# Kernel optimization log

Measured on AMD Instinct MI355X. Metric: run time of the kernel, lower is better.

Reference implementation:

```python
import jax, jax.numpy as jnp
import numpy as np

B, QN, KVN = 4, 512, 512
QD, KD, H, VD = 512, 512, 256, 256


def setup_inputs() -> dict:
    key = jax.random.key(0)
    ks = jax.random.split(key, 6)
    q = jax.random.normal(ks[0], (B, QN, QD), dtype=jnp.float32)
    k = jax.random.normal(ks[1], (B, KVN, KD), dtype=jnp.float32)
    v = jax.random.normal(ks[2], (B, KVN, VD), dtype=jnp.float32)
    # Linear weights (torch nn.Linear stores [out, in]; bias=False)
    Wq = jax.random.normal(ks[3], (H, QD), dtype=jnp.float32) / np.sqrt(QD)
    Wk = jax.random.normal(ks[4], (H, KD), dtype=jnp.float32) / np.sqrt(KD)
    wv = jax.random.normal(ks[5], (H,), dtype=jnp.float32) / np.sqrt(H)
    return {"q": q, "k": k, "v": v, "Wq": Wq, "Wk": Wk, "wv": wv}


def reference(q, k, v, Wq, Wk, wv):
    # Project queries and keys to hidden dim H
    qh = jnp.einsum("bqd,hd->bqh", q, Wq)  # [B, QN, H]
    kh = jnp.einsum("bkd,hd->bkh", k, Wk)  # [B, KVN, H]
    # Broadcast add + tanh: [B, QN, KVN, H]
    energy = jnp.tanh(qh[:, :, None, :] + kh[:, None, :, :])
    # Score projection to scalar per (q, kv) pair
    scores = jnp.einsum("bqkh,h->bqk", energy, wv)  # [B, QN, KVN]
    attention = jax.nn.softmax(scores, axis=-1)
    # Dropout omitted (inference mode)
    output = jnp.einsum("bqk,bkv->bqv", attention, v)  # [B, QN, VD]
    return (output, attention)
```

## Files before the change

### kernel.cpp

```cpp
#include <hip/hip_runtime.h>

#define B_ 4
#define QN 512
#define KVN 512
#define QD_ 512
#define H_ 256
#define VD_ 256
#define TOTR 2048

typedef __attribute__((ext_vector_type(8))) short bf16x8;
typedef __attribute__((ext_vector_type(4))) float f32x4;
typedef __attribute__((ext_vector_type(4))) unsigned short u16x4;
typedef unsigned short u16;

__device__ __forceinline__ float rcp_(float x) { return __builtin_amdgcn_rcpf(x); }
__device__ __forceinline__ float ex2_(float x) { return __builtin_amdgcn_exp2f(x); }

__device__ __forceinline__ u16 bf16_rne(float x) {
    unsigned u = __float_as_uint(x);
    unsigned r = u + 0x7FFFu + ((u >> 16) & 1u);
    return (u16)(r >> 16);
}
__device__ __forceinline__ void split2(float x, u16& h, u16& l) {
    h = bf16_rne(x);
    float hf = __uint_as_float((unsigned)h << 16);
    l = bf16_rne(x - hf);
}
__device__ __forceinline__ void split4(float4 a, u16x4& h, u16x4& l) {
    u16 hh, ll;
    split2(a.x, hh, ll); h[0] = hh; l[0] = ll;
    split2(a.y, hh, ll); h[1] = hh; l[1] = ll;
    split2(a.z, hh, ll); h[2] = hh; l[2] = ll;
    split2(a.w, hh, ll); h[3] = hh; l[3] = ll;
}

__global__ __launch_bounds__(256) void prep(const float* __restrict__ q,
                                            const float* __restrict__ k,
                                            const float* __restrict__ Wq,
                                            const float* __restrict__ Wk,
                                            const float* __restrict__ v,
                                            const float* __restrict__ wv,
                                            u16* __restrict__ q_hi, u16* __restrict__ q_lo,
                                            u16* __restrict__ k_hi, u16* __restrict__ k_lo,
                                            u16* __restrict__ w_hi, u16* __restrict__ w_lo,
                                            u16* __restrict__ vt_hi, u16* __restrict__ vt_lo,
                                            float* __restrict__ iwg) {
    __shared__ float ts[64][65];
    const int tid = threadIdx.x;
    if (blockIdx.x < 2304) {
        const int NQ = 2048 * 512 / 4, NW = 256 * 512 / 4;
        int idx = blockIdx.x * 256 + tid;
        const float* src; u16 *dh, *dl; int off;
        if (idx < NQ)               { src = q;  dh = q_hi; dl = q_lo; off = idx; }
        else if (idx < 2 * NQ)      { src = k;  dh = k_hi; dl = k_lo; off = idx - NQ; }
        else if (idx < 2 * NQ + NW) { src = Wq; dh = w_hi; dl = w_lo; off = idx - 2 * NQ; }
        else { src = Wk; dh = w_hi + 256 * 512; dl = w_lo + 256 * 512; off = idx - 2 * NQ - NW; }
        float4 v4 = ((const float4*)src)[off];
        u16x4 h, l;
        split4(v4, h, l);
        *(u16x4*)(dh + off * 4) = h;
        *(u16x4*)(dl + off * 4) = l;
    } else if (blockIdx.x < 2432) {
        int bid = blockIdx.x - 2304;
        int j0 = (bid & 7) * 64, n0 = ((bid >> 3) & 3) * 64, b = bid >> 5;
#pragma unroll
        for (int t = 0; t < 4; ++t) {
            int idx = t * 256 + tid;
            int j = idx >> 4, nq = idx & 15;
            float4 v4 = *(const float4*)(v + ((size_t)b * KVN + j0 + j) * VD_ + n0 + nq * 4);
            *(float4*)&ts[j][nq * 4] = v4;
        }
        __syncthreads();
#pragma unroll
        for (int t = 0; t < 4; ++t) {
            int idx = t * 256 + tid;
            int jq = idx & 15, n = idx >> 4;
            u16x4 h, l;
            u16 hh, ll;
#pragma unroll
            for (int e = 0; e < 4; ++e) {
                split2(ts[jq * 4 + e][n], hh, ll);
                h[e] = hh; l[e] = ll;
            }
            size_t off = ((size_t)b * VD_ + n0 + n) * KVN + j0 + jq * 4;
            *(u16x4*)(vt_hi + off) = h;
            *(u16x4*)(vt_lo + off) = l;
        }
    } else {
        iwg[tid] = rcp_(wv[tid]);
    }
}

__global__ __launch_bounds__(256) void proj_mfma(const u16* __restrict__ q_hi, const u16* __restrict__ q_lo,
                                                 const u16* __restrict__ k_hi, const u16* __restrict__ k_lo,
                                                 const u16* __restrict__ w_hi, const u16* __restrict__ w_lo,
                                                 const float* __restrict__ iwg,
                                                 float* __restrict__ eqw, float* __restrict__ ekT) {
    const int z = blockIdx.z;
    const u16* __restrict__ Ah_g = z ? k_hi : q_hi;
    const u16* __restrict__ Al_g = z ? k_lo : q_lo;
    const u16* __restrict__ Bh_g = w_hi + (size_t)z * H_ * QD_;
    const u16* __restrict__ Bl_g = w_lo + (size_t)z * H_ * QD_;
    __shared__ u16 Ash[4][32][8], Asl[4][32][8], Bsh[4][32][8], Bsl[4][32][8];
    const int tid = threadIdx.x;
    const int wave = tid >> 6, lane = tid & 63;
    const int fl = lane & 15, kg = lane >> 4;
    const int r0 = blockIdx.y * 32, c0 = blockIdx.x * 32;
    const int ar = 16 * (wave & 1), bc = 16 * (wave >> 1);
    const int frow = (tid & 127) >> 2, fkq = tid & 3, fsel = tid >> 7;
    f32x4 acc = {};
    for (int k0 = 0; k0 < QD_; k0 += 32) {
        __syncthreads();
        {
            const u16* as = (fsel ? Al_g : Ah_g) + (size_t)(r0 + frow) * QD_ + k0 + fkq * 8;
            u16* ad = fsel ? &Asl[fkq][frow][0] : &Ash[fkq][frow][0];
            *(uint4*)ad = *(const uint4*)as;
            const u16* bs = (fsel ? Bl_g : Bh_g) + (size_t)(c0 + frow) * QD_ + k0 + fkq * 8;
            u16* bd = fsel ? &Bsl[fkq][frow][0] : &Bsh[fkq][frow][0];
            *(uint4*)bd = *(const uint4*)bs;
        }
        __syncthreads();
        bf16x8 a_h = *(const bf16x8*)&Ash[kg][ar + fl][0];
        bf16x8 a_l = *(const bf16x8*)&Asl[kg][ar + fl][0];
        bf16x8 b_h = *(const bf16x8*)&Bsh[kg][bc + fl][0];
        bf16x8 b_l = *(const bf16x8*)&Bsl[kg][bc + fl][0];
        acc = __builtin_amdgcn_mfma_f32_16x16x32_bf16(a_h, b_h, acc, 0, 0, 0);
        acc = __builtin_amdgcn_mfma_f32_16x16x32_bf16(a_h, b_l, acc, 0, 0, 0);
        acc = __builtin_amdgcn_mfma_f32_16x16x32_bf16(a_l, b_h, acc, 0, 0, 0);
    }
    const float cs = 2.8853900817779268f;
    const int rg = kg * 4;
    if (z == 1) {
        float4 o = {ex2_(acc[0] * cs), ex2_(acc[1] * cs), ex2_(acc[2] * cs), ex2_(acc[3] * cs)};
        *(float4*)(ekT + (size_t)(c0 + bc + fl) * TOTR + r0 + ar + rg) = o;
    } else {
        float iw = iwg[c0 + bc + fl];
#pragma unroll
        for (int r = 0; r < 4; ++r)
            eqw[(size_t)(r0 + ar + rg + r) * H_ + c0 + bc + fl] = ex2_(acc[r] * cs) * iw;
    }
}

__global__ __launch_bounds__(512, 4) void scores_sm(const float* __restrict__ eqw,
                                                    const float* __restrict__ ekT,
                                                    const float* __restrict__ iwg,
                                                    float* __restrict__ attn,
                                                    u16* __restrict__ at_hi,
                                                    u16* __restrict__ at_lo) {
    const int tid = threadIdx.x;
    const int row0 = blockIdx.x * 4;
    const int b = row0 >> 9;
    const int colg = b * KVN + tid;
    float sc[4] = {};
#pragma unroll 2
    for (int ch = 0; ch < 16; ++ch) {
        const int h0 = ch * 16;
        float ekr[16];
#pragma unroll
        for (int t = 0; t < 16; ++t)
            ekr[t] = ekT[(size_t)(h0 + t) * TOTR + colg];
        float4 iw4[4];
#pragma unroll
        for (int g = 0; g < 4; ++g) iw4[g] = *(const float4*)(iwg + h0 + 4 * g);
#pragma unroll
        for (int qq = 0; qq < 4; ++qq) {
            const float* ep = eqw + (size_t)(row0 + qq) * H_ + h0;
            float s = 0.f;
#pragma unroll
            for (int g = 0; g < 4; ++g) {
                float4 e = *(const float4*)(ep + 4 * g);
                float d0 = __builtin_fmaf(ekr[4 * g + 0], e.x, iw4[g].x);
                float d1 = __builtin_fmaf(ekr[4 * g + 1], e.y, iw4[g].y);
                float d2 = __builtin_fmaf(ekr[4 * g + 2], e.z, iw4[g].z);
                float d3 = __builtin_fmaf(ekr[4 * g + 3], e.w, iw4[g].w);
                float ab = d0 * d1, cd = d2 * d3;
                float num = __builtin_fmaf(d0 + d1, cd, (d2 + d3) * ab);
                s = __builtin_fmaf(num, rcp_(ab * cd), s);
            }
            sc[qq] += s;
        }
    }
    __shared__ float red[8][4];
    const int wid = tid >> 6, lane = tid & 63;
    float ev[4];
#pragma unroll
    for (int qq = 0; qq < 4; ++qq)
        ev[qq] = ex2_(sc[qq] * -2.8853900817779268f);
#pragma unroll
    for (int qq = 0; qq < 4; ++qq) {
        float ssum = ev[qq];
#pragma unroll
        for (int d = 1; d < 64; d <<= 1) ssum += __shfl_xor(ssum, d);
        if (lane == 0) red[wid][qq] = ssum;
    }
    __syncthreads();
#pragma unroll
    for (int qq = 0; qq < 4; ++qq) {
        float tot = ((red[0][qq] + red[1][qq]) + (red[2][qq] + red[3][qq])) +
                    ((red[4][qq] + red[5][qq]) + (red[6][qq] + red[7][qq]));
        float a = ev[qq] * rcp_(tot);
        size_t base = (size_t)(row0 + qq) * KVN + tid;
        attn[base] = a;
        u16 h, l;
        split2(a, h, l);
        at_hi[base] = h;
        at_lo[base] = l;
    }
}

__global__ __launch_bounds__(256) void out_mfma(const u16* __restrict__ vt_hi, const u16* __restrict__ vt_lo,
                                                const u16* __restrict__ at_hi, const u16* __restrict__ at_lo,
                                                float* __restrict__ out) {
    const int b = blockIdx.z;
    const u16* __restrict__ Ah_g = vt_hi + (size_t)b * VD_ * KVN;
    const u16* __restrict__ Al_g = vt_lo + (size_t)b * VD_ * KVN;
    const u16* __restrict__ Bh_g = at_hi + (size_t)b * QN * KVN;
    const u16* __restrict__ Bl_g = at_lo + (size_t)b * QN * KVN;
    float* __restrict__ outb = out + (size_t)b * QN * VD_;
    __shared__ u16 Ash[4][32][8], Asl[4][32][8], Bsh[4][32][8], Bsl[4][32][8];
    const int tid = threadIdx.x;
    const int wave = tid >> 6, lane = tid & 63;
    const int fl = lane & 15, kg = lane >> 4;
    const int r0 = blockIdx.y * 32;
    const int c0 = blockIdx.x * 32;
    const int ar = 16 * (wave & 1), bc = 16 * (wave >> 1);
    const int frow = (tid & 127) >> 2, fkq = tid & 3, fsel = tid >> 7;
    f32x4 acc = {};
    for (int k0 = 0; k0 < KVN; k0 += 32) {
        __syncthreads();
        {
            const u16* as = (fsel ? Al_g : Ah_g) + (size_t)(r0 + frow) * KVN + k0 + fkq * 8;
            u16* ad = fsel ? &Asl[fkq][frow][0] : &Ash[fkq][frow][0];
            *(uint4*)ad = *(const uint4*)as;
            const u16* bs = (fsel ? Bl_g : Bh_g) + (size_t)(c0 + frow) * KVN + k0 + fkq * 8;
            u16* bd = fsel ? &Bsl[fkq][frow][0] : &Bsh[fkq][frow][0];
            *(uint4*)bd = *(const uint4*)bs;
        }
        __syncthreads();
        bf16x8 a_h = *(const bf16x8*)&Ash[kg][ar + fl][0];
        bf16x8 a_l = *(const bf16x8*)&Asl[kg][ar + fl][0];
        bf16x8 b_h = *(const bf16x8*)&Bsh[kg][bc + fl][0];
        bf16x8 b_l = *(const bf16x8*)&Bsl[kg][bc + fl][0];
        acc = __builtin_amdgcn_mfma_f32_16x16x32_bf16(a_h, b_h, acc, 0, 0, 0);
        acc = __builtin_amdgcn_mfma_f32_16x16x32_bf16(a_h, b_l, acc, 0, 0, 0);
        acc = __builtin_amdgcn_mfma_f32_16x16x32_bf16(a_l, b_h, acc, 0, 0, 0);
    }
    const int rg = kg * 4;
    float4 o = {acc[0], acc[1], acc[2], acc[3]};
    *(float4*)(outb + (size_t)(c0 + bc + fl) * VD_ + r0 + ar + rg) = o;
}

extern "C" void kernel_launch(void* const* d_in, const int* in_sizes, int n_in,
                              void* d_out, int out_size, void* d_ws, size_t ws_size,
                              hipStream_t stream) {
    const float* q  = (const float*)d_in[0];
    const float* k  = (const float*)d_in[1];
    const float* v  = (const float*)d_in[2];
    const float* Wq = (const float*)d_in[3];
    const float* Wk = (const float*)d_in[4];
    const float* wv = (const float*)d_in[5];
    float* out  = (float*)d_out;
    float* attn = out + (size_t)B_ * QN * VD_;

    float* eqw = (float*)d_ws;
    float* ekT = eqw + (size_t)TOTR * H_;
    float* iwg = ekT + (size_t)H_ * TOTR;
    u16* q_hi = (u16*)(iwg + 256);
    u16* q_lo = q_hi + 2048 * 512;
    u16* k_hi = q_lo + 2048 * 512;
    u16* k_lo = k_hi + 2048 * 512;
    u16* w_hi = k_lo + 2048 * 512;
    u16* w_lo = w_hi + 512 * 512;
    u16* vt_hi = w_lo + 512 * 512;
    u16* vt_lo = vt_hi + (size_t)B_ * VD_ * KVN;
    u16* at_hi = q_hi;
    u16* at_lo = q_lo;

    prep<<<2433, 256, 0, stream>>>(q, k, Wq, Wk, v, wv, q_hi, q_lo, k_hi, k_lo,
                                   w_hi, w_lo, vt_hi, vt_lo, iwg);
    proj_mfma<<<dim3(H_ / 32, 2048 / 32, 2), 256, 0, stream>>>(q_hi, q_lo, k_hi, k_lo,
                                                               w_hi, w_lo, iwg, eqw, ekT);
    scores_sm<<<TOTR / 4, 512, 0, stream>>>(eqw, ekT, iwg, attn, at_hi, at_lo);
    out_mfma<<<dim3(QN / 32, VD_ / 32, B_), 256, 0, stream>>>(vt_hi, vt_lo, at_hi, at_lo, out);
}
```

Before: 74.90 us.

## Vectorize scores kernel with packed f32x2 math over two key columns per thread

Reworks the scores/softmax kernel so each thread handles two adjacent key columns with packed float2 arithmetic (to map onto packed FMA/mul instructions), while each block now covers two query rows with 256 threads instead of four rows with 512. A duplicated reciprocal-weight array is precomputed so it can feed packed ops directly. The aim is to halve the VALU instruction count in the dominant tanh-sum loop. In exchange, per-thread register use rises, the eqw row reuse per ekT load drops from four rows to two, and the reciprocal is still computed as scalar.

```diff
diff --git a/kernel.cpp b/kernel.cpp
--- a/kernel.cpp
+++ b/kernel.cpp
@@ -10,6 +10,7 @@
 
 typedef __attribute__((ext_vector_type(8))) short bf16x8;
 typedef __attribute__((ext_vector_type(4))) float f32x4;
+typedef __attribute__((ext_vector_type(2))) float f32x2;
 typedef __attribute__((ext_vector_type(4))) unsigned short u16x4;
 typedef unsigned short u16;
 
@@ -44,7 +45,8 @@
                                             u16* __restrict__ k_hi, u16* __restrict__ k_lo,
                                             u16* __restrict__ w_hi, u16* __restrict__ w_lo,
                                             u16* __restrict__ vt_hi, u16* __restrict__ vt_lo,
-                                            float* __restrict__ iwg) {
+                                            float* __restrict__ iwg,
+                                            float2* __restrict__ iwp) {
     __shared__ float ts[64][65];
     const int tid = threadIdx.x;
     if (blockIdx.x < 2304) {
@@ -87,7 +89,10 @@
             *(u16x4*)(vt_lo + off) = l;
         }
     } else {
-        iwg[tid] = rcp_(wv[tid]);
+        float r = rcp_(wv[tid]);
+        iwg[tid] = r;
+        float2 p; p.x = r; p.y = r;
+        iwp[tid] = p;
     }
 }
 
@@ -141,71 +146,78 @@
     }
 }
 
-__global__ __launch_bounds__(512, 4) void scores_sm(const float* __restrict__ eqw,
+__device__ __forceinline__ f32x2 quad_pk(const f32x2* ekp, const f32x2* iw2,
+                                         float ea, float eb, float ec, float ed,
+                                         int base, f32x2 acc) {
+    f32x2 d0 = __builtin_elementwise_fma(ekp[base + 0], (f32x2){ea, ea}, iw2[base + 0]);
+    f32x2 d1 = __builtin_elementwise_fma(ekp[base + 1], (f32x2){eb, eb}, iw2[base + 1]);
+    f32x2 d2 = __builtin_elementwise_fma(ekp[base + 2], (f32x2){ec, ec}, iw2[base + 2]);
+    f32x2 d3 = __builtin_elementwise_fma(ekp[base + 3], (f32x2){ed, ed}, iw2[base + 3]);
+    f32x2 ab = d0 * d1, cd = d2 * d3;
+    f32x2 num = __builtin_elementwise_fma(d0 + d1, cd, (d2 + d3) * ab);
+    f32x2 den = ab * cd;
+    f32x2 r = {rcp_(den.x), rcp_(den.y)};
+    return __builtin_elementwise_fma(num, r, acc);
+}
+
+__global__ __launch_bounds__(256, 4) void scores_sm(const float* __restrict__ eqw,
                                                     const float* __restrict__ ekT,
-                                                    const float* __restrict__ iwg,
+                                                    const float2* __restrict__ iwp,
                                                     float* __restrict__ attn,
                                                     u16* __restrict__ at_hi,
                                                     u16* __restrict__ at_lo) {
     const int tid = threadIdx.x;
-    const int row0 = blockIdx.x * 4;
+    const int row0 = blockIdx.x * 2;
     const int b = row0 >> 9;
-    const int colg = b * KVN + tid;
-    float sc[4] = {};
-#pragma unroll 2
-    for (int ch = 0; ch < 16; ++ch) {
-        const int h0 = ch * 16;
-        float ekr[16];
-#pragma unroll
-        for (int t = 0; t < 16; ++t)
-            ekr[t] = ekT[(size_t)(h0 + t) * TOTR + colg];
-        float4 iw4[4];
-#pragma unroll
-        for (int g = 0; g < 4; ++g) iw4[g] = *(const float4*)(iwg + h0 + 4 * g);
-#pragma unroll
-        for (int qq = 0; qq < 4; ++qq) {
-            const float* ep = eqw + (size_t)(row0 + qq) * H_ + h0;
-            float s = 0.f;
-#pragma unroll
-            for (int g = 0; g < 4; ++g) {
-                float4 e = *(const float4*)(ep + 4 * g);
-                float d0 = __builtin_fmaf(ekr[4 * g + 0], e.x, iw4[g].x);
-                float d1 = __builtin_fmaf(ekr[4 * g + 1], e.y, iw4[g].y);
-                float d2 = __builtin_fmaf(ekr[4 * g + 2], e.z, iw4[g].z);
-                float d3 = __builtin_fmaf(ekr[4 * g + 3], e.w, iw4[g].w);
-                float ab = d0 * d1, cd = d2 * d3;
-                float num = __builtin_fmaf(d0 + d1, cd, (d2 + d3) * ab);
-                s = __builtin_fmaf(num, rcp_(ab * cd), s);
-            }
-            sc[qq] += s;
-        }
-    }
-    __shared__ float red[8][4];
+    const float* __restrict__ ekcol = ekT + b * KVN + 2 * tid;
+    f32x2 sc0 = {0.f, 0.f}, sc1 = {0.f, 0.f};
+    for (int ch = 0; ch < 32; ++ch) {
+        const int h0 = ch * 8;
+        f32x2 ekp[8], iw2[8];
+#pragma unroll
+        for (int t = 0; t < 8; ++t) {
+            ekp[t] = *(const f32x2*)(ekcol + (size_t)(h0 + t) * TOTR);
+            float2 w = iwp[h0 + t];
+            iw2[t].x = w.x; iw2[t].y = w.y;
+        }
+        const float* ep0 = eqw + (size_t)row0 * H_ + h0;
+        const float* ep1 = ep0 + H_;
+#pragma unroll
+        for (int g = 0; g < 2; ++g) {
+            float4 e0 = *(const float4*)(ep0 + 4 * g);
+            float4 e1 = *(const float4*)(ep1 + 4 * g);
+            sc0 = quad_pk(ekp, iw2, e0.x, e0.y, e0.z, e0.w, 4 * g, sc0);
+            sc1 = quad_pk(ekp, iw2, e1.x, e1.y, e1.z, e1.w, 4 * g, sc1);
+        }
+    }
+    __shared__ float red[4][2];
     const int wid = tid >> 6, lane = tid & 63;
-    float ev[4];
-#pragma unroll
-    for (int qq = 0; qq < 4; ++qq)
-        ev[qq] = ex2_(sc[qq] * -2.8853900817779268f);
-#pragma unroll
-    for (int qq = 0; qq < 4; ++qq) {
-        float ssum = ev[qq];
-#pragma unroll
-        for (int d = 1; d < 64; d <<= 1) ssum += __shfl_xor(ssum, d);
-        if (lane == 0) red[wid][qq] = ssum;
-    }
+    const float cexp = -2.8853900817779268f;
+    f32x2 ev0 = {ex2_(sc0.x * cexp), ex2_(sc0.y * cexp)};
+    f32x2 ev1 = {ex2_(sc1.x * cexp), ex2_(sc1.y * cexp)};
+    float s0 = ev0.x + ev0.y, s1 = ev1.x + ev1.y;
+#pragma unroll
+    for (int d = 1; d < 64; d <<= 1) {
+        s0 += __shfl_xor(s0, d);
+        s1 += __shfl_xor(s1, d);
+    }
+    if (lane == 0) { red[wid][0] = s0; red[wid][1] = s1; }
     __syncthreads();
-#pragma unroll
-    for (int qq = 0; qq < 4; ++qq) {
-        float tot = ((red[0][qq] + red[1][qq]) + (red[2][qq] + red[3][qq])) +
-                    ((red[4][qq] + red[5][qq]) + (red[6][qq] + red[7][qq]));
-        float a = ev[qq] * rcp_(tot);
-        size_t base = (size_t)(row0 + qq) * KVN + tid;
-        attn[base] = a;
-        u16 h, l;
-        split2(a, h, l);
-        at_hi[base] = h;
-        at_lo[base] = l;
-    }
+    float i0 = rcp_(red[0][0] + red[1][0] + red[2][0] + red[3][0]);
+    float i1 = rcp_(red[0][1] + red[1][1] + red[2][1] + red[3][1]);
+    size_t base0 = (size_t)row0 * KVN + 2 * tid;
+    size_t base1 = base0 + KVN;
+    f32x2 a0 = {ev0.x * i0, ev0.y * i0};
+    f32x2 a1 = {ev1.x * i1, ev1.y * i1};
+    *(f32x2*)(attn + base0) = a0;
+    *(f32x2*)(attn + base1) = a1;
+    u16 h0v, l0v, h1v, l1v;
+    split2(a0.x, h0v, l0v); split2(a0.y, h1v, l1v);
+    *(uint*)(at_hi + base0) = (uint)h0v | ((uint)h1v << 16);
+    *(uint*)(at_lo + base0) = (uint)l0v | ((uint)l1v << 16);
+    split2(a1.x, h0v, l0v); split2(a1.y, h1v, l1v);
+    *(uint*)(at_hi + base1) = (uint)h0v | ((uint)h1v << 16);
+    *(uint*)(at_lo + base1) = (uint)l0v | ((uint)l1v << 16);
 }
 
 __global__ __launch_bounds__(256) void out_mfma(const u16* __restrict__ vt_hi, const u16* __restrict__ vt_lo,
@@ -265,7 +277,8 @@
     float* eqw = (float*)d_ws;
     float* ekT = eqw + (size_t)TOTR * H_;
     float* iwg = ekT + (size_t)H_ * TOTR;
-    u16* q_hi = (u16*)(iwg + 256);
+    float2* iwp = (float2*)(iwg + 256);
+    u16* q_hi = (u16*)(iwp + 256);
     u16* q_lo = q_hi + 2048 * 512;
     u16* k_hi = q_lo + 2048 * 512;
     u16* k_lo = k_hi + 2048 * 512;
@@ -277,9 +290,9 @@
     u16* at_lo = q_lo;
 
     prep<<<2433, 256, 0, stream>>>(q, k, Wq, Wk, v, wv, q_hi, q_lo, k_hi, k_lo,
-                                   w_hi, w_lo, vt_hi, vt_lo, iwg);
+                                   w_hi, w_lo, vt_hi, vt_lo, iwg, iwp);
     proj_mfma<<<dim3(H_ / 32, 2048 / 32, 2), 256, 0, stream>>>(q_hi, q_lo, k_hi, k_lo,
                                                                w_hi, w_lo, iwg, eqw, ekT);
-    scores_sm<<<TOTR / 4, 512, 0, stream>>>(eqw, ekT, iwg, attn, at_hi, at_lo);
+    scores_sm<<<TOTR / 2, 256, 0, stream>>>(eqw, ekT, iwp, attn, at_hi, at_lo);
     out_mfma<<<dim3(QN / 32, VD_ / 32, B_), 256, 0, stream>>>(vt_hi, vt_lo, at_hi, at_lo, out);
 }
```

After: 70.78 us. 1.06x faster.
